# Performance work log

Hardware: AMD Instinct MI355X
Metric: run time of the kernel (lower is better)

Reference implementation:

```python
import jax, jax.numpy as jnp
import numpy as np


def setup_inputs() -> dict:
    key = jax.random.key(0)
    k1, k2 = jax.random.split(key)
    B, L, D = 8, 4096, 1024
    hidden = jax.random.normal(k1, (B, L, D), dtype=jnp.float32)
    w1 = jax.random.normal(k2, (D // 2 + 1,), dtype=jnp.float32)
    return {"hidden": hidden, "w1": w1}


def reference(hidden, w1):
    # hidden: [B, L, D]; w1: [D//2+1]
    B, L, D = hidden.shape
    flat = hidden.reshape(-1, D)                 # [B*L, D]
    Xf1 = jnp.fft.rfft(flat, axis=1)             # [B*L, D//2+1] complex
    gate = jax.nn.softmax(w1, axis=0)[None, :]   # [1, D//2+1]
    t1 = jnp.fft.irfft(Xf1 * gate, n=D, axis=1)  # [B*L, D]
    return t1.reshape(B, L, D).astype(hidden.dtype)
```

## Files before the change

### kernel.cpp

```cpp
#include <hip/hip_runtime.h>


#define R2F 0.70710678118654752f

template <bool INV>
__device__ __forceinline__ void bfly8(float* xr, float* xi)
{
    float t0r = xr[0] + xr[4], t0i = xi[0] + xi[4];
    float t1r = xr[0] - xr[4], t1i = xi[0] - xi[4];
    float t2r = xr[2] + xr[6], t2i = xi[2] + xi[6];
    float t3r = xr[2] - xr[6], t3i = xi[2] - xi[6];
    float e0r = t0r + t2r, e0i = t0i + t2i;
    float e2r = t0r - t2r, e2i = t0i - t2i;
    float e1r, e1i, e3r, e3i;
    if (!INV) { e1r = t1r + t3i; e1i = t1i - t3r; e3r = t1r - t3i; e3i = t1i + t3r; }
    else      { e1r = t1r - t3i; e1i = t1i + t3r; e3r = t1r + t3i; e3i = t1i - t3r; }
    float s0r = xr[1] + xr[5], s0i = xi[1] + xi[5];
    float s1r = xr[1] - xr[5], s1i = xi[1] - xi[5];
    float s2r = xr[3] + xr[7], s2i = xi[3] + xi[7];
    float s3r = xr[3] - xr[7], s3i = xi[3] - xi[7];
    float o0r = s0r + s2r, o0i = s0i + s2i;
    float o2r = s0r - s2r, o2i = s0i - s2i;
    float o1r, o1i, o3r, o3i;
    if (!INV) { o1r = s1r + s3i; o1i = s1i - s3r; o3r = s1r - s3i; o3i = s1i + s3r; }
    else      { o1r = s1r - s3i; o1i = s1i + s3r; o3r = s1r + s3i; o3i = s1i - s3r; }
    float p1r, p1i, p2r, p2i, p3r, p3i;
    if (!INV) {
        p1r = (o1r + o1i) * R2F;  p1i = (o1i - o1r) * R2F;
        p2r = o2i;                p2i = -o2r;
        p3r = (o3i - o3r) * R2F;  p3i = -(o3r + o3i) * R2F;
    } else {
        p1r = (o1r - o1i) * R2F;  p1i = (o1i + o1r) * R2F;
        p2r = -o2i;               p2i = o2r;
        p3r = -(o3r + o3i) * R2F; p3i = (o3r - o3i) * R2F;
    }
    xr[0] = e0r + o0r; xi[0] = e0i + o0i;
    xr[4] = e0r - o0r; xi[4] = e0i - o0i;
    xr[1] = e1r + p1r; xi[1] = e1i + p1i;
    xr[5] = e1r - p1r; xi[5] = e1i - p1i;
    xr[2] = e2r + p2r; xi[2] = e2i + p2i;
    xr[6] = e2r - p2r; xi[6] = e2i - p2i;
    xr[3] = e3r + p3r; xi[3] = e3i + p3i;
    xr[7] = e3r - p3r; xi[7] = e3i - p3i;
}

template <bool INV>
__device__ __forceinline__ void tw_apply(float* xr, float* xi,
                                         const float* c, const float* s)
{
#pragma unroll
    for (int k = 1; k < 8; ++k) {
        float r, i;
        if (!INV) { r = xr[k] * c[k] + xi[k] * s[k]; i = xi[k] * c[k] - xr[k] * s[k]; }
        else      { r = xr[k] * c[k] - xi[k] * s[k]; i = xi[k] * c[k] + xr[k] * s[k]; }
        xr[k] = r; xi[k] = i;
    }
}

__global__ __launch_bounds__(256)
void fv_kernel(const float2* __restrict__ x,
               const float2* __restrict__ pq,
               const float2* __restrict__ tw1,
               const float2* __restrict__ tw8,
               float2* __restrict__ out)
{
    __shared__ float sre[4][544], sim[4][544];
    const int tid = threadIdx.x;
    const int r = tid >> 6;
    const int t = tid & 63;
    float* re = sre[r]; float* im = sim[r];
    const size_t rowbase = ((size_t)blockIdx.x * 4 + r) * 512;

    float c1[8], s1[8], c8[8], s8[8];
#pragma unroll
    for (int k = 1; k < 8; ++k) {
        float2 w = tw1[(k - 1) * 64 + t];        c1[k] = w.x; s1[k] = w.y;
        float2 v = tw8[(k - 1) * 8 + (t >> 3)];  c8[k] = v.x; s8[k] = v.y;
    }

    const int p0 = (t << 3) + (t >> 1);
    const int lt = t + (t >> 4);
    const int sb = (t & 7) + 68 * (t >> 3);

    float zr[8], zi[8];

#pragma unroll
    for (int k = 0; k < 8; ++k) {
        float2 v = x[rowbase + t + 64 * k];
        zr[k] = v.x; zi[k] = v.y;
    }
    bfly8<false>(zr, zi);
    tw_apply<false>(zr, zi, c1, s1);
#pragma unroll
    for (int k = 0; k < 8; ++k) { re[p0 + k] = zr[k]; im[p0 + k] = zi[k]; }
#pragma unroll
    for (int k = 0; k < 8; ++k) { zr[k] = re[lt + 68 * k]; zi[k] = im[lt + 68 * k]; }
    bfly8<false>(zr, zi);
    tw_apply<false>(zr, zi, c8, s8);
#pragma unroll
    for (int k = 0; k < 8; ++k) {
        int a = sb + 8 * k + (k >> 1);
        re[a] = zr[k]; im[a] = zi[k];
    }
#pragma unroll
    for (int k = 0; k < 8; ++k) { zr[k] = re[lt + 68 * k]; zi[k] = im[lt + 68 * k]; }
    bfly8<false>(zr, zi);

    {
        const int src = (64 - t) & 63;
        float vr[8], vi[8];
#pragma unroll
        for (int k = 0; k < 8; ++k) {
            vr[k] = __shfl(zr[7 - k], src, 64);
            vi[k] = __shfl(zi[7 - k], src, 64);
        }
        if (t == 0) {
#pragma unroll
            for (int k = 0; k < 8; ++k) {
                int kk = (8 - k) & 7;
                vr[k] = zr[kk]; vi[k] = zi[kk];
            }
        }
#pragma unroll
        for (int k = 0; k < 8; ++k) {
            float2 g = pq[t + 64 * k];
            float nr = g.x * zr[k] + g.y * vi[k];
            float ni = g.x * zi[k] + g.y * vr[k];
            zr[k] = nr; zi[k] = ni;
        }
    }

    bfly8<true>(zr, zi);
    tw_apply<true>(zr, zi, c1, s1);
#pragma unroll
    for (int k = 0; k < 8; ++k) { re[p0 + k] = zr[k]; im[p0 + k] = zi[k]; }
#pragma unroll
    for (int k = 0; k < 8; ++k) { zr[k] = re[lt + 68 * k]; zi[k] = im[lt + 68 * k]; }
    bfly8<true>(zr, zi);
    tw_apply<true>(zr, zi, c8, s8);
#pragma unroll
    for (int k = 0; k < 8; ++k) {
        int a = sb + 8 * k + (k >> 1);
        re[a] = zr[k]; im[a] = zi[k];
    }
#pragma unroll
    for (int k = 0; k < 8; ++k) { zr[k] = re[lt + 68 * k]; zi[k] = im[lt + 68 * k]; }
    bfly8<true>(zr, zi);
#pragma unroll
    for (int k = 0; k < 8; ++k) {
        out[rowbase + t + 64 * k] = make_float2(zr[k], zi[k]);
    }
}

__global__ void gate_kernel(const float* __restrict__ w1,
                            float2* __restrict__ pq,
                            float2* __restrict__ tw1,
                            float2* __restrict__ tw8)
{
    __shared__ float red[1024];
    __shared__ float ex[513];
    const int t = threadIdx.x;

    float v = (t < 513) ? w1[t] : -1e30f;
    red[t] = v;
    __syncthreads();
    for (int off = 512; off > 0; off >>= 1) {
        if (t < off) red[t] = fmaxf(red[t], red[t + off]);
        __syncthreads();
    }
    float M = red[0];
    __syncthreads();

    float e = (t < 513) ? expf(w1[t] - M) : 0.0f;
    if (t < 513) ex[t] = e;
    red[t] = e;
    __syncthreads();
    for (int off = 512; off > 0; off >>= 1) {
        if (t < off) red[t] += red[t + off];
        __syncthreads();
    }
    float inv = 1.0f / red[0];
    __syncthreads();

    if (t < 512) {
        float ga = ex[t] * inv;
        float gb = ex[512 - t] * inv;
        float gp = ga + gb, gm = ga - gb;
        float th = (float)t * 6.13592315154256492e-03f;
        float sn, cs;
        __sincosf(th, &sn, &cs);
        float P = 0.5f * (gp - gm * sn) * (1.0f / 512.0f);
        float q = 0.5f * (gm * cs) * (1.0f / 512.0f);
        pq[t] = make_float2(P, q);
    }
    if (t < 448) {
        int k = (t >> 6) + 1;
        int j = t & 63;
        float th = (float)(j * k) * 1.22718463151036952e-02f;
        float sn, cs;
        sincosf(th, &sn, &cs);
        tw1[t] = make_float2(cs, sn);
    }
    if (t < 56) {
        int k = (t >> 3) + 1;
        int p = t & 7;
        float th = (float)(p * k) * 9.81747704246810387e-02f;
        float sn, cs;
        sincosf(th, &sn, &cs);
        tw8[t] = make_float2(cs, sn);
    }
}

extern "C" void kernel_launch(void* const* d_in, const int* in_sizes, int n_in,
                              void* d_out, int out_size, void* d_ws, size_t ws_size,
                              hipStream_t stream)
{
    (void)n_in; (void)out_size; (void)ws_size;
    const float2* hidden = (const float2*)d_in[0];
    const float*  w1     = (const float*)d_in[1];
    float2* out = (float2*)d_out;

    float2* pq  = (float2*)d_ws;
    float2* tw1 = pq + 512;
    float2* tw8 = tw1 + 448;

    gate_kernel<<<1, 1024, 0, stream>>>(w1, pq, tw1, tw8);

    const int rows   = in_sizes[0] / 1024;
    const int blocks = rows / 4;
    fv_kernel<<<blocks, 256, 0, stream>>>(hidden, pq, tw1, tw8, out);
}
```

Baseline: 235.4 us.

## Process two rows per wavefront with interleaved float2 shared-memory FFT stages

```diff
diff --git a/kernel.cpp b/kernel.cpp
--- a/kernel.cpp
+++ b/kernel.cpp
@@ -57,19 +57,19 @@
     }
 }
 
-__global__ __launch_bounds__(256)
+__global__ __launch_bounds__(256, 4)
 void fv_kernel(const float2* __restrict__ x,
                const float2* __restrict__ pq,
                const float2* __restrict__ tw1,
                const float2* __restrict__ tw8,
                float2* __restrict__ out)
 {
-    __shared__ float sre[4][544], sim[4][544];
+    __shared__ float2 sz[8][568];
     const int tid = threadIdx.x;
     const int r = tid >> 6;
     const int t = tid & 63;
-    float* re = sre[r]; float* im = sim[r];
-    const size_t rowbase = ((size_t)blockIdx.x * 4 + r) * 512;
+    float2* shrow[2] = { sz[2 * r], sz[2 * r + 1] };
+    const size_t base0 = ((size_t)blockIdx.x * 8 + 2 * r) * 512;
 
     float c1[8], s1[8], c8[8], s8[8];
 #pragma unroll
@@ -79,76 +79,116 @@
     }
 
     const int p0 = (t << 3) + (t >> 1);
-    const int lt = t + (t >> 4);
-    const int sb = (t & 7) + 68 * (t >> 3);
-
-    float zr[8], zi[8];
-
-#pragma unroll
-    for (int k = 0; k < 8; ++k) {
-        float2 v = x[rowbase + t + 64 * k];
-        zr[k] = v.x; zi[k] = v.y;
-    }
-    bfly8<false>(zr, zi);
-    tw_apply<false>(zr, zi, c1, s1);
-#pragma unroll
-    for (int k = 0; k < 8; ++k) { re[p0 + k] = zr[k]; im[p0 + k] = zi[k]; }
-#pragma unroll
-    for (int k = 0; k < 8; ++k) { zr[k] = re[lt + 68 * k]; zi[k] = im[lt + 68 * k]; }
-    bfly8<false>(zr, zi);
-    tw_apply<false>(zr, zi, c8, s8);
-#pragma unroll
-    for (int k = 0; k < 8; ++k) {
-        int a = sb + 8 * k + (k >> 1);
-        re[a] = zr[k]; im[a] = zi[k];
-    }
-#pragma unroll
-    for (int k = 0; k < 8; ++k) { zr[k] = re[lt + 68 * k]; zi[k] = im[lt + 68 * k]; }
-    bfly8<false>(zr, zi);
-
-    {
+    const int l1 = t + (t >> 4);
+    const int s2 = (t & 7) + 72 * (t >> 3);
+
+    float zr[2][8], zi[2][8];
+
+#pragma unroll
+    for (int rr = 0; rr < 2; ++rr)
+#pragma unroll
+        for (int k = 0; k < 8; ++k) {
+            float2 v = x[base0 + 512 * rr + t + 64 * k];
+            zr[rr][k] = v.x; zi[rr][k] = v.y;
+        }
+
+#pragma unroll
+    for (int rr = 0; rr < 2; ++rr) {
+        bfly8<false>(zr[rr], zi[rr]);
+        tw_apply<false>(zr[rr], zi[rr], c1, s1);
+        float2* sh = shrow[rr];
+#pragma unroll
+        for (int k = 0; k < 8; ++k) sh[p0 + k] = make_float2(zr[rr][k], zi[rr][k]);
+    }
+#pragma unroll
+    for (int rr = 0; rr < 2; ++rr) {
+        float2* sh = shrow[rr];
+#pragma unroll
+        for (int k = 0; k < 8; ++k) {
+            float2 v = sh[l1 + 68 * k]; zr[rr][k] = v.x; zi[rr][k] = v.y;
+        }
+    }
+#pragma unroll
+    for (int rr = 0; rr < 2; ++rr) {
+        bfly8<false>(zr[rr], zi[rr]);
+        tw_apply<false>(zr[rr], zi[rr], c8, s8);
+        float2* sh = shrow[rr];
+#pragma unroll
+        for (int k = 0; k < 8; ++k) sh[s2 + 8 * k] = make_float2(zr[rr][k], zi[rr][k]);
+    }
+#pragma unroll
+    for (int rr = 0; rr < 2; ++rr) {
+        float2* sh = shrow[rr];
+#pragma unroll
+        for (int k = 0; k < 8; ++k) {
+            float2 v = sh[t + 72 * k]; zr[rr][k] = v.x; zi[rr][k] = v.y;
+        }
+    }
+
+#pragma unroll
+    for (int rr = 0; rr < 2; ++rr) {
+        bfly8<false>(zr[rr], zi[rr]);
         const int src = (64 - t) & 63;
         float vr[8], vi[8];
 #pragma unroll
         for (int k = 0; k < 8; ++k) {
-            vr[k] = __shfl(zr[7 - k], src, 64);
-            vi[k] = __shfl(zi[7 - k], src, 64);
+            vr[k] = __shfl(zr[rr][7 - k], src, 64);
+            vi[k] = __shfl(zi[rr][7 - k], src, 64);
         }
         if (t == 0) {
 #pragma unroll
             for (int k = 0; k < 8; ++k) {
                 int kk = (8 - k) & 7;
-                vr[k] = zr[kk]; vi[k] = zi[kk];
+                vr[k] = zr[rr][kk]; vi[k] = zi[rr][kk];
             }
         }
 #pragma unroll
         for (int k = 0; k < 8; ++k) {
             float2 g = pq[t + 64 * k];
-            float nr = g.x * zr[k] + g.y * vi[k];
-            float ni = g.x * zi[k] + g.y * vr[k];
-            zr[k] = nr; zi[k] = ni;
-        }
-    }
-
-    bfly8<true>(zr, zi);
-    tw_apply<true>(zr, zi, c1, s1);
-#pragma unroll
-    for (int k = 0; k < 8; ++k) { re[p0 + k] = zr[k]; im[p0 + k] = zi[k]; }
-#pragma unroll
-    for (int k = 0; k < 8; ++k) { zr[k] = re[lt + 68 * k]; zi[k] = im[lt + 68 * k]; }
-    bfly8<true>(zr, zi);
-    tw_apply<true>(zr, zi, c8, s8);
-#pragma unroll
-    for (int k = 0; k < 8; ++k) {
-        int a = sb + 8 * k + (k >> 1);
-        re[a] = zr[k]; im[a] = zi[k];
-    }
-#pragma unroll
-    for (int k = 0; k < 8; ++k) { zr[k] = re[lt + 68 * k]; zi[k] = im[lt + 68 * k]; }
-    bfly8<true>(zr, zi);
-#pragma unroll
-    for (int k = 0; k < 8; ++k) {
-        out[rowbase + t + 64 * k] = make_float2(zr[k], zi[k]);
+            float nr = g.x * zr[rr][k] + g.y * vi[k];
+            float ni = g.x * zi[rr][k] + g.y * vr[k];
+            zr[rr][k] = nr; zi[rr][k] = ni;
+        }
+    }
+
+#pragma unroll
+    for (int rr = 0; rr < 2; ++rr) {
+        bfly8<true>(zr[rr], zi[rr]);
+        tw_apply<true>(zr[rr], zi[rr], c1, s1);
+        float2* sh = shrow[rr];
+#pragma unroll
+        for (int k = 0; k < 8; ++k) sh[p0 + k] = make_float2(zr[rr][k], zi[rr][k]);
+    }
+#pragma unroll
+    for (int rr = 0; rr < 2; ++rr) {
+        float2* sh = shrow[rr];
+#pragma unroll
+        for (int k = 0; k < 8; ++k) {
+            float2 v = sh[l1 + 68 * k]; zr[rr][k] = v.x; zi[rr][k] = v.y;
+        }
+    }
+#pragma unroll
+    for (int rr = 0; rr < 2; ++rr) {
+        bfly8<true>(zr[rr], zi[rr]);
+        tw_apply<true>(zr[rr], zi[rr], c8, s8);
+        float2* sh = shrow[rr];
+#pragma unroll
+        for (int k = 0; k < 8; ++k) sh[s2 + 8 * k] = make_float2(zr[rr][k], zi[rr][k]);
+    }
+#pragma unroll
+    for (int rr = 0; rr < 2; ++rr) {
+        float2* sh = shrow[rr];
+#pragma unroll
+        for (int k = 0; k < 8; ++k) {
+            float2 v = sh[t + 72 * k]; zr[rr][k] = v.x; zi[rr][k] = v.y;
+        }
+    }
+#pragma unroll
+    for (int rr = 0; rr < 2; ++rr) {
+        bfly8<true>(zr[rr], zi[rr]);
+#pragma unroll
+        for (int k = 0; k < 8; ++k)
+            out[base0 + 512 * rr + t + 64 * k] = make_float2(zr[rr][k], zi[rr][k]);
     }
 }
 
@@ -227,6 +267,6 @@
     gate_kernel<<<1, 1024, 0, stream>>>(w1, pq, tw1, tw8);
 
     const int rows   = in_sizes[0] / 1024;
-    const int blocks = rows / 4;
+    const int blocks = rows / 8;
     fv_kernel<<<blocks, 256, 0, stream>>>(hidden, pq, tw1, tw8, out);
 }
```

After: 244.4 us. 1.04x slower.

## Process four rows per wave with register prefetch and interleaved float2 LDS

Applied to the files above, without the earlier changes.

```diff
diff --git a/kernel.cpp b/kernel.cpp
--- a/kernel.cpp
+++ b/kernel.cpp
@@ -57,6 +57,8 @@
     }
 }
 
+#define ROWS_PER_WAVE 4
+
 __global__ __launch_bounds__(256)
 void fv_kernel(const float2* __restrict__ x,
                const float2* __restrict__ pq,
@@ -64,12 +66,13 @@
                const float2* __restrict__ tw8,
                float2* __restrict__ out)
 {
-    __shared__ float sre[4][544], sim[4][544];
+    __shared__ float2 sz[4][568];
     const int tid = threadIdx.x;
     const int r = tid >> 6;
     const int t = tid & 63;
-    float* re = sre[r]; float* im = sim[r];
-    const size_t rowbase = ((size_t)blockIdx.x * 4 + r) * 512;
+    float2* sh = sz[r];
+    const size_t wavebase =
+        ((size_t)blockIdx.x * (4 * ROWS_PER_WAVE) + r * ROWS_PER_WAVE) * 512;
 
     float c1[8], s1[8], c8[8], s8[8];
 #pragma unroll
@@ -79,76 +82,92 @@
     }
 
     const int p0 = (t << 3) + (t >> 1);
-    const int lt = t + (t >> 4);
-    const int sb = (t & 7) + 68 * (t >> 3);
-
-    float zr[8], zi[8];
-
-#pragma unroll
-    for (int k = 0; k < 8; ++k) {
-        float2 v = x[rowbase + t + 64 * k];
-        zr[k] = v.x; zi[k] = v.y;
-    }
-    bfly8<false>(zr, zi);
-    tw_apply<false>(zr, zi, c1, s1);
-#pragma unroll
-    for (int k = 0; k < 8; ++k) { re[p0 + k] = zr[k]; im[p0 + k] = zi[k]; }
-#pragma unroll
-    for (int k = 0; k < 8; ++k) { zr[k] = re[lt + 68 * k]; zi[k] = im[lt + 68 * k]; }
-    bfly8<false>(zr, zi);
-    tw_apply<false>(zr, zi, c8, s8);
-#pragma unroll
-    for (int k = 0; k < 8; ++k) {
-        int a = sb + 8 * k + (k >> 1);
-        re[a] = zr[k]; im[a] = zi[k];
-    }
-#pragma unroll
-    for (int k = 0; k < 8; ++k) { zr[k] = re[lt + 68 * k]; zi[k] = im[lt + 68 * k]; }
-    bfly8<false>(zr, zi);
-
-    {
-        const int src = (64 - t) & 63;
-        float vr[8], vi[8];
-#pragma unroll
-        for (int k = 0; k < 8; ++k) {
-            vr[k] = __shfl(zr[7 - k], src, 64);
-            vi[k] = __shfl(zi[7 - k], src, 64);
-        }
-        if (t == 0) {
+    const int l1 = t + (t >> 4);
+    const int s2 = (t & 7) + 72 * (t >> 3);
+
+    const int src = (64 - t) & 63;
+
+    float2 cur[8], nxt[8];
+#pragma unroll
+    for (int k = 0; k < 8; ++k) cur[k] = x[wavebase + t + 64 * k];
+
+    for (int i = 0; i < ROWS_PER_WAVE; ++i) {
+        if (i < ROWS_PER_WAVE - 1) {
+            const size_t nb = wavebase + (size_t)(i + 1) * 512;
+#pragma unroll
+            for (int k = 0; k < 8; ++k) nxt[k] = x[nb + t + 64 * k];
+        }
+
+        float zr[8], zi[8];
+#pragma unroll
+        for (int k = 0; k < 8; ++k) { zr[k] = cur[k].x; zi[k] = cur[k].y; }
+
+        bfly8<false>(zr, zi);
+        tw_apply<false>(zr, zi, c1, s1);
+#pragma unroll
+        for (int k = 0; k < 8; ++k) sh[p0 + k] = make_float2(zr[k], zi[k]);
+#pragma unroll
+        for (int k = 0; k < 8; ++k) {
+            float2 v = sh[l1 + 68 * k]; zr[k] = v.x; zi[k] = v.y;
+        }
+        bfly8<false>(zr, zi);
+        tw_apply<false>(zr, zi, c8, s8);
+#pragma unroll
+        for (int k = 0; k < 8; ++k) sh[s2 + 8 * k] = make_float2(zr[k], zi[k]);
+#pragma unroll
+        for (int k = 0; k < 8; ++k) {
+            float2 v = sh[t + 72 * k]; zr[k] = v.x; zi[k] = v.y;
+        }
+        bfly8<false>(zr, zi);
+
+        {
+            float vr[8], vi[8];
 #pragma unroll
             for (int k = 0; k < 8; ++k) {
-                int kk = (8 - k) & 7;
-                vr[k] = zr[kk]; vi[k] = zi[kk];
+                vr[k] = __shfl(zr[7 - k], src, 64);
+                vi[k] = __shfl(zi[7 - k], src, 64);
             }
-        }
-#pragma unroll
-        for (int k = 0; k < 8; ++k) {
-            float2 g = pq[t + 64 * k];
-            float nr = g.x * zr[k] + g.y * vi[k];
-            float ni = g.x * zi[k] + g.y * vr[k];
-            zr[k] = nr; zi[k] = ni;
-        }
-    }
-
-    bfly8<true>(zr, zi);
-    tw_apply<true>(zr, zi, c1, s1);
-#pragma unroll
-    for (int k = 0; k < 8; ++k) { re[p0 + k] = zr[k]; im[p0 + k] = zi[k]; }
-#pragma unroll
-    for (int k = 0; k < 8; ++k) { zr[k] = re[lt + 68 * k]; zi[k] = im[lt + 68 * k]; }
-    bfly8<true>(zr, zi);
-    tw_apply<true>(zr, zi, c8, s8);
-#pragma unroll
-    for (int k = 0; k < 8; ++k) {
-        int a = sb + 8 * k + (k >> 1);
-        re[a] = zr[k]; im[a] = zi[k];
-    }
-#pragma unroll
-    for (int k = 0; k < 8; ++k) { zr[k] = re[lt + 68 * k]; zi[k] = im[lt + 68 * k]; }
-    bfly8<true>(zr, zi);
-#pragma unroll
-    for (int k = 0; k < 8; ++k) {
-        out[rowbase + t + 64 * k] = make_float2(zr[k], zi[k]);
+            if (t == 0) {
+#pragma unroll
+                for (int k = 0; k < 8; ++k) {
+                    int kk = (8 - k) & 7;
+                    vr[k] = zr[kk]; vi[k] = zi[kk];
+                }
+            }
+#pragma unroll
+            for (int k = 0; k < 8; ++k) {
+                float2 g = pq[t + 64 * k];
+                float nr = g.x * zr[k] + g.y * vi[k];
+                float ni = g.x * zi[k] + g.y * vr[k];
+                zr[k] = nr; zi[k] = ni;
+            }
+        }
+
+        bfly8<true>(zr, zi);
+        tw_apply<true>(zr, zi, c1, s1);
+#pragma unroll
+        for (int k = 0; k < 8; ++k) sh[p0 + k] = make_float2(zr[k], zi[k]);
+#pragma unroll
+        for (int k = 0; k < 8; ++k) {
+            float2 v = sh[l1 + 68 * k]; zr[k] = v.x; zi[k] = v.y;
+        }
+        bfly8<true>(zr, zi);
+        tw_apply<true>(zr, zi, c8, s8);
+#pragma unroll
+        for (int k = 0; k < 8; ++k) sh[s2 + 8 * k] = make_float2(zr[k], zi[k]);
+#pragma unroll
+        for (int k = 0; k < 8; ++k) {
+            float2 v = sh[t + 72 * k]; zr[k] = v.x; zi[k] = v.y;
+        }
+        bfly8<true>(zr, zi);
+
+        const size_t ob = wavebase + (size_t)i * 512;
+#pragma unroll
+        for (int k = 0; k < 8; ++k)
+            out[ob + t + 64 * k] = make_float2(zr[k], zi[k]);
+
+#pragma unroll
+        for (int k = 0; k < 8; ++k) cur[k] = nxt[k];
     }
 }
 
@@ -227,6 +246,6 @@
     gate_kernel<<<1, 1024, 0, stream>>>(w1, pq, tw1, tw8);
 
     const int rows   = in_sizes[0] / 1024;
-    const int blocks = rows / 4;
+    const int blocks = rows / (4 * ROWS_PER_WAVE);
     fv_kernel<<<blocks, 256, 0, stream>>>(hidden, pq, tw1, tw8, out);
 }
```

After: 238.9 us. About the same (+1.5%).

## Process two rows per wavefront with float4 LDS exchange and LDS-based mirror

Applied to the files above, without the earlier changes.

```diff
diff --git a/kernel.cpp b/kernel.cpp
--- a/kernel.cpp
+++ b/kernel.cpp
@@ -64,12 +64,13 @@
                const float2* __restrict__ tw8,
                float2* __restrict__ out)
 {
-    __shared__ float sre[4][544], sim[4][544];
+    __shared__ float4 sb4[4][576];
     const int tid = threadIdx.x;
     const int r = tid >> 6;
     const int t = tid & 63;
-    float* re = sre[r]; float* im = sim[r];
-    const size_t rowbase = ((size_t)blockIdx.x * 4 + r) * 512;
+    float4* buf = sb4[r];
+    const size_t baseA = ((size_t)blockIdx.x * 8 + 2 * r) * 512;
+    const size_t baseB = baseA + 512;
 
     float c1[8], s1[8], c8[8], s8[8];
 #pragma unroll
@@ -78,78 +79,91 @@
         float2 v = tw8[(k - 1) * 8 + (t >> 3)];  c8[k] = v.x; s8[k] = v.y;
     }
 
-    const int p0 = (t << 3) + (t >> 1);
-    const int lt = t + (t >> 4);
-    const int sb = (t & 7) + 68 * (t >> 3);
-
-    float zr[8], zi[8];
-
-#pragma unroll
-    for (int k = 0; k < 8; ++k) {
-        float2 v = x[rowbase + t + 64 * k];
-        zr[k] = v.x; zi[k] = v.y;
-    }
-    bfly8<false>(zr, zi);
-    tw_apply<false>(zr, zi, c1, s1);
-#pragma unroll
-    for (int k = 0; k < 8; ++k) { re[p0 + k] = zr[k]; im[p0 + k] = zi[k]; }
-#pragma unroll
-    for (int k = 0; k < 8; ++k) { zr[k] = re[lt + 68 * k]; zi[k] = im[lt + 68 * k]; }
-    bfly8<false>(zr, zi);
-    tw_apply<false>(zr, zi, c8, s8);
-#pragma unroll
-    for (int k = 0; k < 8; ++k) {
-        int a = sb + 8 * k + (k >> 1);
-        re[a] = zr[k]; im[a] = zi[k];
-    }
-#pragma unroll
-    for (int k = 0; k < 8; ++k) { zr[k] = re[lt + 68 * k]; zi[k] = im[lt + 68 * k]; }
-    bfly8<false>(zr, zi);
-
-    {
-        const int src = (64 - t) & 63;
-        float vr[8], vi[8];
-#pragma unroll
-        for (int k = 0; k < 8; ++k) {
-            vr[k] = __shfl(zr[7 - k], src, 64);
-            vi[k] = __shfl(zi[7 - k], src, 64);
-        }
-        if (t == 0) {
-#pragma unroll
-            for (int k = 0; k < 8; ++k) {
-                int kk = (8 - k) & 7;
-                vr[k] = zr[kk]; vi[k] = zi[kk];
-            }
-        }
-#pragma unroll
-        for (int k = 0; k < 8; ++k) {
-            float2 g = pq[t + 64 * k];
-            float nr = g.x * zr[k] + g.y * vi[k];
-            float ni = g.x * zi[k] + g.y * vr[k];
-            zr[k] = nr; zi[k] = ni;
-        }
-    }
-
-    bfly8<true>(zr, zi);
-    tw_apply<true>(zr, zi, c1, s1);
-#pragma unroll
-    for (int k = 0; k < 8; ++k) { re[p0 + k] = zr[k]; im[p0 + k] = zi[k]; }
-#pragma unroll
-    for (int k = 0; k < 8; ++k) { zr[k] = re[lt + 68 * k]; zi[k] = im[lt + 68 * k]; }
-    bfly8<true>(zr, zi);
-    tw_apply<true>(zr, zi, c8, s8);
-#pragma unroll
-    for (int k = 0; k < 8; ++k) {
-        int a = sb + 8 * k + (k >> 1);
-        re[a] = zr[k]; im[a] = zi[k];
-    }
-#pragma unroll
-    for (int k = 0; k < 8; ++k) { zr[k] = re[lt + 68 * k]; zi[k] = im[lt + 68 * k]; }
-    bfly8<true>(zr, zi);
-#pragma unroll
-    for (int k = 0; k < 8; ++k) {
-        out[rowbase + t + 64 * k] = make_float2(zr[k], zi[k]);
-    }
+    const int st1 = 9 * t;
+    const int ld0 = t + (t >> 3);
+    const int st2 = (t & 7) + 72 * (t >> 3);
+
+    float ar[8], ai[8], br[8], bi[8];
+    float pqx[8], pqy[8];
+
+#pragma unroll
+    for (int k = 0; k < 8; ++k) {
+        float2 g = pq[t + 64 * k];
+        pqx[k] = g.x; pqy[k] = g.y;
+    }
+
+#pragma unroll
+    for (int k = 0; k < 8; ++k) {
+        float2 v = x[baseA + t + 64 * k];
+        ar[k] = v.x; ai[k] = v.y;
+    }
+#pragma unroll
+    for (int k = 0; k < 8; ++k) {
+        float2 v = x[baseB + t + 64 * k];
+        br[k] = v.x; bi[k] = v.y;
+    }
+
+    bfly8<false>(ar, ai); tw_apply<false>(ar, ai, c1, s1);
+    bfly8<false>(br, bi); tw_apply<false>(br, bi, c1, s1);
+#pragma unroll
+    for (int k = 0; k < 8; ++k) buf[st1 + k] = make_float4(ar[k], ai[k], br[k], bi[k]);
+#pragma unroll
+    for (int k = 0; k < 8; ++k) {
+        float4 v = buf[ld0 + 72 * k];
+        ar[k] = v.x; ai[k] = v.y; br[k] = v.z; bi[k] = v.w;
+    }
+    bfly8<false>(ar, ai); tw_apply<false>(ar, ai, c8, s8);
+    bfly8<false>(br, bi); tw_apply<false>(br, bi, c8, s8);
+#pragma unroll
+    for (int k = 0; k < 8; ++k) buf[st2 + 9 * k] = make_float4(ar[k], ai[k], br[k], bi[k]);
+#pragma unroll
+    for (int k = 0; k < 8; ++k) {
+        float4 v = buf[ld0 + 72 * k];
+        ar[k] = v.x; ai[k] = v.y; br[k] = v.z; bi[k] = v.w;
+    }
+    bfly8<false>(ar, ai);
+    bfly8<false>(br, bi);
+
+#pragma unroll
+    for (int k = 0; k < 8; ++k) buf[ld0 + 72 * k] = make_float4(ar[k], ai[k], br[k], bi[k]);
+#pragma unroll
+    for (int k = 0; k < 8; ++k) {
+        int m = (512 - (t + 64 * k)) & 511;
+        float4 v = buf[m + (m >> 3)];
+        float nrA = pqx[k] * ar[k] + pqy[k] * v.y;
+        float niA = pqx[k] * ai[k] + pqy[k] * v.x;
+        float nrB = pqx[k] * br[k] + pqy[k] * v.w;
+        float niB = pqx[k] * bi[k] + pqy[k] * v.z;
+        ar[k] = nrA; ai[k] = niA; br[k] = nrB; bi[k] = niB;
+    }
+
+    bfly8<true>(ar, ai); tw_apply<true>(ar, ai, c1, s1);
+    bfly8<true>(br, bi); tw_apply<true>(br, bi, c1, s1);
+#pragma unroll
+    for (int k = 0; k < 8; ++k) buf[st1 + k] = make_float4(ar[k], ai[k], br[k], bi[k]);
+#pragma unroll
+    for (int k = 0; k < 8; ++k) {
+        float4 v = buf[ld0 + 72 * k];
+        ar[k] = v.x; ai[k] = v.y; br[k] = v.z; bi[k] = v.w;
+    }
+    bfly8<true>(ar, ai); tw_apply<true>(ar, ai, c8, s8);
+    bfly8<true>(br, bi); tw_apply<true>(br, bi, c8, s8);
+#pragma unroll
+    for (int k = 0; k < 8; ++k) buf[st2 + 9 * k] = make_float4(ar[k], ai[k], br[k], bi[k]);
+#pragma unroll
+    for (int k = 0; k < 8; ++k) {
+        float4 v = buf[ld0 + 72 * k];
+        ar[k] = v.x; ai[k] = v.y; br[k] = v.z; bi[k] = v.w;
+    }
+    bfly8<true>(ar, ai);
+    bfly8<true>(br, bi);
+
+#pragma unroll
+    for (int k = 0; k < 8; ++k)
+        out[baseA + t + 64 * k] = make_float2(ar[k], ai[k]);
+#pragma unroll
+    for (int k = 0; k < 8; ++k)
+        out[baseB + t + 64 * k] = make_float2(br[k], bi[k]);
 }
 
 __global__ void gate_kernel(const float* __restrict__ w1,
@@ -227,6 +241,6 @@
     gate_kernel<<<1, 1024, 0, stream>>>(w1, pq, tw1, tw8);
 
     const int rows   = in_sizes[0] / 1024;
-    const int blocks = rows / 4;
+    const int blocks = rows / 8;
     fv_kernel<<<blocks, 256, 0, stream>>>(hidden, pq, tw1, tw8, out);
 }
```

Result: no change. 236.4 us (+0.5%).
